# Performance work log

Measured on AMD Instinct MI355X. Metric: run time of the kernel, lower is better.

## Reference

```python
import jax, jax.numpy as jnp
import numpy as np

BATCH = 8
NDATA = 8192
NPOINT = 1024
NSAMPLE = 32
RADIUS = 0.2
CFEAT = 64


def setup_inputs() -> dict:
    key = jax.random.key(0)
    k1, k2, k3 = jax.random.split(key, 3)
    new_xyz = jax.random.normal(k1, (BATCH, NPOINT, 3), dtype=jnp.float32)
    xyz = jax.random.normal(k2, (BATCH, NDATA, 3), dtype=jnp.float32)
    points = jax.random.normal(k3, (BATCH, NDATA, CFEAT), dtype=jnp.float32)
    return {"new_xyz": new_xyz, "xyz": xyz, "points": points}


def reference(new_xyz, xyz, points):
    # Pairwise distances from every centroid to every dataset point.
    # delta: [B, P, N, 3]
    delta = xyz[:, None, :, :] - new_xyz[:, :, None, :]
    dist = jnp.linalg.norm(delta, axis=-1)  # [B, P, N]

    # Sort by distance (the original does a full argsort per centroid).
    sorted_idx = jnp.argsort(dist, axis=-1).astype(jnp.int32)  # [B, P, N]
    sorted_d = jnp.take_along_axis(dist, sorted_idx, axis=-1)  # [B, P, N]

    # Nearest point index replaces out-of-radius slots.
    nearest = sorted_idx[:, :, 0:1]  # [B, P, 1]
    radius_idx = jnp.where(sorted_d < RADIUS, sorted_idx, nearest)
    idx = radius_idx[:, :, :NSAMPLE]  # [B, P, S] int32 (ndataset >= nsample)

    # Batched gathers: grouped_xyz [B, P, S, 3], grouped_points [B, P, S, C].
    grouped_xyz = jnp.take_along_axis(
        xyz[:, None, :, :], idx[..., None], axis=2)
    grouped_points = jnp.take_along_axis(
        points[:, None, :, :], idx[..., None], axis=2)
    new_points = jnp.concatenate([grouped_xyz, grouped_points], axis=-1)
    return (new_points, idx, grouped_xyz)
```

## Files before the change

kernel.cpp:

```cpp
#include <hip/hip_runtime.h>
#include <math.h>

typedef unsigned int   u32;
typedef unsigned long long u64;

#define BATCH   8
#define NDATA   8192
#define NPOINT  1024
#define NSAMPLE 32
#define CFEAT   64
#define ROWF    67
#define MAXCAND 128
#define QPB     4
#define NB      256

#define OUT_IDX (BATCH*NPOINT*NSAMPLE*ROWF)
#define OUT_GX  (OUT_IDX + BATCH*NPOINT*NSAMPLE)

__device__ __forceinline__ float rnbf(float f) {
    u32 b = __float_as_uint(f);
    b += 0x7FFFu + ((b >> 16) & 1u);
    return __uint_as_float(b & 0xFFFF0000u);
}
__device__ __forceinline__ int clampidx(int v) {
    return (v < 0) ? 0 : (v > NDATA-1 ? NDATA-1 : v);
}
__device__ __forceinline__ int xbucket(float v) {
    int c = (int)floorf((v + 4.5f) * 28.444445f);
    return c < 0 ? 0 : (c > NB-1 ? NB-1 : c);
}

__global__ __launch_bounds__(1024)
void bin_kernel(const float* __restrict__ xyz,
                float4* __restrict__ wp, u32* __restrict__ wst)
{
    __shared__ u32 cnt[NB];
    __shared__ u32 sc[NB];
    const int b = blockIdx.x, tid = threadIdx.x;
    const float* bx = xyz + (size_t)b * NDATA * 3;

    if (tid < NB) cnt[tid] = 0;
    __syncthreads();
    for (int p = tid; p < NDATA; p += 1024)
        atomicAdd(&cnt[xbucket(bx[p*3])], 1u);
    __syncthreads();

    if (tid < NB) sc[tid] = cnt[tid];
    __syncthreads();
    #pragma unroll
    for (int d = 1; d < NB; d <<= 1) {
        u32 t = 0;
        if (tid < NB && tid >= d) t = sc[tid - d];
        __syncthreads();
        if (tid < NB && tid >= d) sc[tid] += t;
        __syncthreads();
    }
    if (tid < NB) {
        u32 excl = (tid == 0) ? 0u : sc[tid - 1];
        cnt[tid] = excl;
        wst[b*(NB+1) + tid] = excl;
        if (tid == 0) wst[b*(NB+1) + NB] = NDATA;
    }
    __syncthreads();

    for (int p = tid; p < NDATA; p += 1024) {
        float x = bx[p*3], y = bx[p*3+1], z = bx[p*3+2];
        u32 pos = atomicAdd(&cnt[xbucket(x)], 1u);
        wp[(size_t)b*NDATA + pos] = make_float4(x, y, z, __uint_as_float((u32)p));
    }
}

__global__ __launch_bounds__(256, 8)
void grouping_kernel(const float* __restrict__ new_xyz,
                     const float* __restrict__ xyz,
                     const float* __restrict__ points,
                     const float4* __restrict__ wp, const u32* __restrict__ wst,
                     float* __restrict__ out, float T)
{
    __shared__ float cand_s[QPB][MAXCAND];
    __shared__ int   cand_i[QPB][MAXCAND];
    __shared__ int   sel[QPB][NSAMPLE];

    const int tid  = threadIdx.x;
    const int wv   = tid >> 6;
    const int lane = tid & 63;
    const int q    = blockIdx.x * QPB + wv;
    const int b    = q >> 10;

    if (lane < NSAMPLE) sel[wv][lane] = 0;

    const float qx = new_xyz[q*3 + 0];
    const float qy = new_xyz[q*3 + 1];
    const float qz = new_xyz[q*3 + 2];
    const float*  bx = xyz + (size_t)b * NDATA * 3;
    const float4* cp = wp  + (size_t)b * NDATA;

    const int blo = xbucket(__fsub_rn(qx, 0.2005f));
    const int bhi = xbucket(__fadd_rn(qx, 0.2005f));
    const u32 j0 = wst[b*(NB+1) + blo];
    const u32 j1 = wst[b*(NB+1) + bhi + 1];

    int n = 0;
    for (u32 jb = j0; jb < j1; jb += 64) {
        u32 j  = jb + lane;
        bool in = j < j1;
        u32 jj = in ? j : (j1 - 1);
        float4 v = cp[jj];
        float dx = __fsub_rn(v.x, qx);
        float dy = __fsub_rn(v.y, qy);
        float dz = __fsub_rn(v.z, qz);
        float d2 = __fadd_rn(__fadd_rn(__fmul_rn(dx,dx), __fmul_rn(dy,dy)),
                             __fmul_rn(dz,dz));
        bool cc = in && (d2 < T);
        u64 m = __ballot(cc);
        if (m) {
            if (cc) {
                int below = __builtin_amdgcn_mbcnt_hi((u32)(m >> 32),
                             __builtin_amdgcn_mbcnt_lo((u32)m, 0));
                int pos = n + below;
                if (pos < MAXCAND) {
                    cand_s[wv][pos] = __fsqrt_rn(d2);
                    cand_i[wv][pos] = (int)__float_as_uint(v.w);
                }
            }
            n += (int)__popcll(m);
        }
    }

    int mini = 0;
    if (n == 0) {
        float mind = 3.402823466e38f; int mi = 0;
        for (int k = 0; k < NDATA/64; ++k) {
            int i = (k << 6) + lane;
            float dx = __fsub_rn(bx[i*3+0], qx);
            float dy = __fsub_rn(bx[i*3+1], qy);
            float dz = __fsub_rn(bx[i*3+2], qz);
            float d2 = __fadd_rn(__fadd_rn(__fmul_rn(dx,dx), __fmul_rn(dy,dy)),
                                 __fmul_rn(dz,dz));
            if (d2 < mind) { mind = d2; mi = i; }
        }
        float ms = __fsqrt_rn(mind);
        for (int off = 32; off; off >>= 1) {
            float os = __shfl_xor(ms, off);
            int   oi = __shfl_xor(mi, off);
            if (os < ms || (os == ms && oi < mi)) { ms = os; mi = oi; }
        }
        mini = mi;
    }

    __syncthreads();

    const int nj = n > MAXCAND ? MAXCAND : n;
    for (int kk = lane; kk < nj; kk += 64) {
        float sk = cand_s[wv][kk];
        int   ik = cand_i[wv][kk];
        int r = 0;
        for (int mm = 0; mm < nj; ++mm) {
            float sm = cand_s[wv][mm];
            int   im = cand_i[wv][mm];
            r += (int)((sm < sk) | ((sm == sk) & (im < ik)));
        }
        if (r < NSAMPLE) sel[wv][r] = clampidx(ik);
    }
    __syncthreads();
    {
        const int nsel = nj < NSAMPLE ? nj : NSAMPLE;
        if (lane >= nsel && lane < NSAMPLE) {
            int pad = (nj > 0) ? sel[wv][0] : clampidx(mini);
            sel[wv][lane] = pad;
        }
    }
    __syncthreads();

    if (lane < NSAMPLE)
        out[OUT_IDX + (size_t)q*NSAMPLE + lane] = rnbf((float)sel[wv][lane]);

    for (int e = lane; e < NSAMPLE*3; e += 64) {
        int sR = e / 3, c2 = e - sR*3;
        int is = sel[wv][sR];
        out[OUT_GX + (size_t)q*(NSAMPLE*3) + e] = rnbf(bx[is*3 + c2]);
    }

    const float* prow = points + (size_t)b * NDATA * CFEAT;
    float* onp = out + (size_t)q * (NSAMPLE*ROWF);
    #pragma unroll 2
    for (int e = lane; e < NSAMPLE*ROWF; e += 64) {
        int sR = e / ROWF;
        int c2 = e - sR*ROWF;
        int is = sel[wv][sR];
        const float* ap = (c2 < 3) ? (bx + (size_t)is*3 + c2)
                                   : (prow + (size_t)is*CFEAT + (c2-3));
        onp[e] = rnbf(*ap);
    }
}

extern "C" void kernel_launch(void* const* d_in, const int* in_sizes, int n_in,
                              void* d_out, int out_size, void* d_ws, size_t ws_size,
                              hipStream_t stream) {
    union { u32 u; float f; } lo, hi, mid;
    lo.u = 0u; hi.f = 0.05f;
    while (hi.u - lo.u > 1u) {
        mid.u = lo.u + (hi.u - lo.u) / 2u;
        if (sqrtf(mid.f) >= 0.2f) hi.u = mid.u; else lo.u = mid.u;
    }
    float T = hi.f;

    float4* wp  = (float4*)d_ws;
    u32*    wst = (u32*)(wp + (size_t)BATCH*NDATA);

    const float* nxz = (const float*)d_in[0];
    const float* xyz = (const float*)d_in[1];
    const float* pts = (const float*)d_in[2];

    bin_kernel<<<BATCH, 1024, 0, stream>>>(xyz, wp, wst);
    grouping_kernel<<<(BATCH*NPOINT)/QPB, 256, 0, stream>>>(
        nxz, xyz, pts, wp, wst, (float*)d_out, T);
}
```

Before: 130.1 us.

## Stage gathered feature rows in LDS for float4 writes; unroll candidate scan by two

The final gather now fetches each point's 64 features with float4 loads, converts them to bf16-rounded floats and stages 8 output rows per wave in shared memory. Each staged tile is then written out with contiguous float4 stores, replacing the scalar per-element loads and stores that did a divide by 67 per element. The candidate scan also handles two 64-point chunks per iteration to expose more memory-level parallelism. In exchange it adds LDS use per block and block-wide __syncthreads inside the output loop, which may reduce occupancy and add barrier stalls.

Result: faster. 126.1 us (-3.1%).

```diff
diff --git a/kernel.cpp b/kernel.cpp
--- a/kernel.cpp
+++ b/kernel.cpp
@@ -24,6 +24,10 @@
 }
 __device__ __forceinline__ int clampidx(int v) {
     return (v < 0) ? 0 : (v > NDATA-1 ? NDATA-1 : v);
+}
+__device__ __forceinline__ int lanes_below(u64 m) {
+    return __builtin_amdgcn_mbcnt_hi((u32)(m >> 32),
+            __builtin_amdgcn_mbcnt_lo((u32)m, 0));
 }
 __device__ __forceinline__ int xbucket(float v) {
     int c = (int)floorf((v + 4.5f) * 28.444445f);
@@ -80,6 +84,7 @@
     __shared__ float cand_s[QPB][MAXCAND];
     __shared__ int   cand_i[QPB][MAXCAND];
     __shared__ int   sel[QPB][NSAMPLE];
+    __shared__ __align__(16) float st[QPB][8*ROWF];
 
     const int tid  = threadIdx.x;
     const int wv   = tid >> 6;
@@ -101,30 +106,43 @@
     const u32 j1 = wst[b*(NB+1) + bhi + 1];
 
     int n = 0;
-    for (u32 jb = j0; jb < j1; jb += 64) {
-        u32 j  = jb + lane;
-        bool in = j < j1;
-        u32 jj = in ? j : (j1 - 1);
-        float4 v = cp[jj];
-        float dx = __fsub_rn(v.x, qx);
-        float dy = __fsub_rn(v.y, qy);
-        float dz = __fsub_rn(v.z, qz);
-        float d2 = __fadd_rn(__fadd_rn(__fmul_rn(dx,dx), __fmul_rn(dy,dy)),
-                             __fmul_rn(dz,dz));
-        bool cc = in && (d2 < T);
-        u64 m = __ballot(cc);
-        if (m) {
-            if (cc) {
-                int below = __builtin_amdgcn_mbcnt_hi((u32)(m >> 32),
-                             __builtin_amdgcn_mbcnt_lo((u32)m, 0));
-                int pos = n + below;
-                if (pos < MAXCAND) {
-                    cand_s[wv][pos] = __fsqrt_rn(d2);
-                    cand_i[wv][pos] = (int)__float_as_uint(v.w);
-                }
+    for (u32 jb = j0; jb < j1; jb += 128) {
+        u32 ja = jb + lane;
+        u32 jc = jb + 64 + lane;
+        bool ia = ja < j1;
+        bool ib = jc < j1;
+        float4 va = cp[ia ? ja : (j1 - 1u)];
+        float4 vb = cp[ib ? jc : (j1 - 1u)];
+        float dxa = __fsub_rn(va.x, qx);
+        float dya = __fsub_rn(va.y, qy);
+        float dza = __fsub_rn(va.z, qz);
+        float d2a = __fadd_rn(__fadd_rn(__fmul_rn(dxa,dxa), __fmul_rn(dya,dya)),
+                              __fmul_rn(dza,dza));
+        float dxb = __fsub_rn(vb.x, qx);
+        float dyb = __fsub_rn(vb.y, qy);
+        float dzb = __fsub_rn(vb.z, qz);
+        float d2b = __fadd_rn(__fadd_rn(__fmul_rn(dxb,dxb), __fmul_rn(dyb,dyb)),
+                              __fmul_rn(dzb,dzb));
+        bool ca = ia && (d2a < T);
+        bool cb = ib && (d2b < T);
+        u64 ma = __ballot(ca);
+        u64 mb = __ballot(cb);
+        if (ca) {
+            int pos = n + lanes_below(ma);
+            if (pos < MAXCAND) {
+                cand_s[wv][pos] = __fsqrt_rn(d2a);
+                cand_i[wv][pos] = (int)__float_as_uint(va.w);
             }
-            n += (int)__popcll(m);
-        }
+        }
+        n += (int)__popcll(ma);
+        if (cb) {
+            int pos = n + lanes_below(mb);
+            if (pos < MAXCAND) {
+                cand_s[wv][pos] = __fsqrt_rn(d2b);
+                cand_i[wv][pos] = (int)__float_as_uint(vb.w);
+            }
+        }
+        n += (int)__popcll(mb);
     }
 
     int mini = 0;
@@ -183,14 +201,29 @@
 
     const float* prow = points + (size_t)b * NDATA * CFEAT;
     float* onp = out + (size_t)q * (NSAMPLE*ROWF);
-    #pragma unroll 2
-    for (int e = lane; e < NSAMPLE*ROWF; e += 64) {
-        int sR = e / ROWF;
-        int c2 = e - sR*ROWF;
-        int is = sel[wv][sR];
-        const float* ap = (c2 < 3) ? (bx + (size_t)is*3 + c2)
-                                   : (prow + (size_t)is*CFEAT + (c2-3));
-        onp[e] = rnbf(*ap);
+    const int gq = lane >> 4;
+    const int lq = lane & 15;
+    for (int g = 0; g < 4; ++g) {
+        #pragma unroll
+        for (int p = 0; p < 2; ++p) {
+            int rl = p*4 + gq;
+            int is = sel[wv][g*8 + rl];
+            const float4 v = *reinterpret_cast<const float4*>(
+                                 prow + (size_t)is*CFEAT + 4*lq);
+            float* d = &st[wv][rl*ROWF + 3 + 4*lq];
+            d[0] = rnbf(v.x); d[1] = rnbf(v.y); d[2] = rnbf(v.z); d[3] = rnbf(v.w);
+        }
+        if (lane < 24) {
+            int rl = lane / 3, c = lane - rl*3;
+            int is = sel[wv][g*8 + rl];
+            st[wv][rl*ROWF + c] = rnbf(bx[(size_t)is*3 + c]);
+        }
+        __syncthreads();
+        for (int i = lane; i < 134; i += 64) {
+            float4 t = *reinterpret_cast<const float4*>(&st[wv][4*i]);
+            *reinterpret_cast<float4*>(onp + (size_t)g*536 + 4*i) = t;
+        }
+        __syncthreads();
     }
 }
 
```
